# Optimization experiments

Hardware: AMD Instinct MI355X
Metric: run time of the kernel (lower is better)

The kernel has to match this reference:

```python
import jax, jax.numpy as jnp
import numpy as np

N_NODES = 100000
N_EDGES = 1600000
N_FEAT = 16
HIDDEN = 128
N_GRAPHS = 512


def setup_inputs() -> dict:
    key = jax.random.key(0)
    ks = jax.random.split(key, 9)
    x = jax.random.normal(ks[0], (N_NODES, N_FEAT), dtype=jnp.float32)
    edge_index = jax.random.randint(ks[1], (2, N_EDGES), 0, N_NODES, dtype=jnp.int64)
    batch = jnp.sort(jax.random.randint(ks[2], (N_NODES,), 0, N_GRAPHS, dtype=jnp.int64))
    s1 = 1.0 / np.sqrt(N_FEAT)
    s2 = 1.0 / np.sqrt(HIDDEN)
    W1 = jax.random.uniform(ks[3], (N_FEAT, HIDDEN), jnp.float32, -s1, s1)
    b1 = jax.random.uniform(ks[4], (HIDDEN,), jnp.float32, -s1, s1)
    W2 = jax.random.uniform(ks[5], (HIDDEN, HIDDEN), jnp.float32, -s2, s2)
    b2 = jax.random.uniform(ks[6], (HIDDEN,), jnp.float32, -s2, s2)
    Wl = jax.random.uniform(ks[7], (HIDDEN, 1), jnp.float32, -s2, s2)
    bl = jax.random.uniform(ks[8], (1,), jnp.float32, -s2, s2)
    return {"x": x, "edge_index": edge_index, "batch": batch,
            "W1": W1, "b1": b1, "W2": W2, "b2": b2, "Wl": Wl, "bl": bl}


def _gcn_conv(x, W, b, src, dst, n_nodes):
    # PyG GCNConv: h = x @ W; add self-loops; sym-normalized scatter-add; + bias
    h = x @ W  # [N, H]
    deg = jnp.zeros((n_nodes,), h.dtype).at[dst].add(1.0) + 1.0  # self-loop adds 1
    dinv = jax.lax.rsqrt(deg)  # deg >= 1, safe
    norm = dinv[src] * dinv[dst]  # [E]
    out = jnp.zeros_like(h).at[dst].add(h[src] * norm[:, None])
    out = out + h * (dinv * dinv)[:, None]  # self-loop term
    return out + b


def reference(x, edge_index, batch, W1, b1, W2, b2, Wl, bl):
    src, dst = edge_index[0], edge_index[1]
    n = x.shape[0]
    h = jax.nn.relu(_gcn_conv(x, W1, b1, src, dst, n))
    h = jax.nn.relu(_gcn_conv(h, W2, b2, src, dst, n))
    # global_mean_pool over graphs
    sums = jax.ops.segment_sum(h, batch, num_segments=N_GRAPHS)
    counts = jax.ops.segment_sum(jnp.ones((n,), h.dtype), batch, num_segments=N_GRAPHS)
    pooled = sums / jnp.maximum(counts, 1.0)[:, None]  # [G, H]
    return (pooled @ Wl + bl).squeeze(-1)  # [G]
```

## Files before the change

### kernel.cpp

```cpp
#include <hip/hip_runtime.h>
#include <hip/hip_bf16.h>

#define N_NODES 100000
#define N_EDGES 1600000
#define N_FEAT  16
#define HIDDEN  128
#define N_GRAPHS 512
#define CAP     64
#define NBKT    782
#define BN      128
#define CAPB    2560
#define EPB     4000

typedef unsigned short ushort_t;
typedef short v8s __attribute__((ext_vector_type(8)));
typedef float v4f __attribute__((ext_vector_type(4)));

__device__ __forceinline__ ushort_t f2bf(float f) {
    __hip_bfloat16 b = __float2bfloat16(f);
    return *(ushort_t*)&b;
}
__device__ __forceinline__ float bf_lo(unsigned u) {
    union { unsigned i; float f; } c; c.i = u << 16; return c.f;
}
__device__ __forceinline__ float bf_hi(unsigned u) {
    union { unsigned i; float f; } c; c.i = u & 0xffff0000u; return c.f;
}


__global__ __launch_bounds__(256) void k_part(const int* __restrict__ src,
                                              const int* __restrict__ dst,
                                              int* __restrict__ bcnt,
                                              int* __restrict__ ebuf,
                                              const float* __restrict__ W2,
                                              ushort_t* __restrict__ Bp) {
    int tid = threadIdx.x;

    if (blockIdx.x >= N_EDGES / EPB) {
        int idx = (blockIdx.x - N_EDGES / EPB) * 256 + tid;
        int j = idx & 7;
        int lane = (idx >> 3) & 63;
        int nt = (idx >> 9) & 7;
        int kt = idx >> 12;
        int k = kt * 32 + (lane >> 4) * 8 + j;
        int n = nt * 16 + (lane & 15);
        Bp[idx] = f2bf(W2[k * HIDDEN + n]);
        return;
    }

    __shared__ int h[NBKT];
    __shared__ int base[NBKT];
    __shared__ int r[NBKT];
    int e0 = blockIdx.x * EPB;

    for (int i = tid; i < NBKT; i += 256) { h[i] = 0; r[i] = 0; }
    __syncthreads();

    int nloc = (tid < EPB - 15 * 256) ? 16 : 15;
    int v[16], bb[16];
    #pragma unroll
    for (int k = 0; k < 16; ++k) {
        if (k < nloc) {
            int i = e0 + tid + k * 256;
            int s = src[i], d = dst[i];
            bb[k] = d >> 7;
            v[k] = s | ((d & 127) << 17);
            atomicAdd(&h[bb[k]], 1);
        }
    }
    __syncthreads();

    for (int i = tid; i < NBKT; i += 256)
        base[i] = atomicAdd(&bcnt[i], h[i]);
    __syncthreads();

    #pragma unroll
    for (int k = 0; k < 16; ++k) {
        if (k < nloc) {
            int b = bb[k];
            int pos = base[b] + atomicAdd(&r[b], 1);
            if (pos < CAPB) ebuf[b * CAPB + pos] = v[k];
        }
    }
}


__global__ __launch_bounds__(256) void k_fill(const int* __restrict__ bcnt,
                                              const int* __restrict__ ebuf,
                                              const float* __restrict__ x,
                                              int* __restrict__ esrc64,
                                              int* __restrict__ cnt,
                                              float* __restrict__ dinv,
                                              ushort_t* __restrict__ xb,
                                              ushort_t* __restrict__ h1) {
    __shared__ int lcnt[BN];
    int tid = threadIdx.x;
    int b = blockIdx.x;
    int node0 = b << 7;

    if (tid < BN) lcnt[tid] = 0;
    __syncthreads();

    int nE = bcnt[b]; nE = nE > CAPB ? CAPB : nE;
    const int* eb = ebuf + b * CAPB;
    for (int i = tid; i < nE; i += 256) {
        int v = eb[i];
        int dl = v >> 17;
        int p = atomicAdd(&lcnt[dl], 1);
        if (p < CAP) esrc64[((node0 + dl) << 6) + p] = v & 0x1FFFF;
    }
    __syncthreads();

    if (tid < BN) {
        int node = node0 + tid;
        if (node < N_NODES) {
            int c = lcnt[tid];
            cnt[node] = c;
            dinv[node] = rsqrtf((float)c + 1.0f);
            int cc = c > CAP ? CAP : c;
            int pad = (cc + 7) & ~7;
            for (int p = cc; p < pad; ++p)
                esrc64[(node << 6) + p] = N_NODES;
        }
    }

    for (int i = tid; i < BN * N_FEAT; i += 256) {
        int nl = i >> 4;
        int node = node0 + nl;
        if (node < N_NODES) {
            float di = rsqrtf((float)lcnt[nl] + 1.0f);
            xb[node * N_FEAT + (i & 15)] = f2bf(x[node * N_FEAT + (i & 15)] * di);
        }
    }

    if (b == 0) {
        if (tid < N_FEAT) xb[N_NODES * N_FEAT + tid] = 0;
        if (tid < HIDDEN) h1[(size_t)N_NODES * HIDDEN + tid] = 0;
    }
}


__global__ __launch_bounds__(256) void k_agg1f(const int* __restrict__ cnt,
                                               const int* __restrict__ esrc64,
                                               const float* __restrict__ dinv,
                                               const ushort_t* __restrict__ xb,
                                               const float* __restrict__ W1,
                                               const float* __restrict__ b1,
                                               ushort_t* __restrict__ h1) {
    __shared__ float sw[N_FEAT * HIDDEN];
    __shared__ float sx[32][20];
    __shared__ float sdd[32];
    int tid = threadIdx.x;
    for (int i = tid; i < N_FEAT * HIDDEN; i += 256) sw[i] = W1[i];

    int wv = tid >> 6;
    int sub = (tid >> 3) & 7;
    int l8 = tid & 7;
    int nl = wv * 8 + sub;
    int node = blockIdx.x * 32 + nl;
    const unsigned* xr = (const unsigned*)xb;

    int deg = cnt[node]; deg = deg > CAP ? CAP : deg;
    int deg8 = (deg + 7) & ~7;
    int base = node << 6;
    float dd = dinv[node];

    float a0 = 0.0f, a1 = 0.0f;
    for (int j = 0; j < deg8; j += 8) {
        int4 ia = *(const int4*)(esrc64 + base + j);
        int4 ib = *(const int4*)(esrc64 + base + j + 4);
        unsigned u0 = xr[(unsigned)ia.x * 8 + l8];
        unsigned u1 = xr[(unsigned)ia.y * 8 + l8];
        unsigned u2 = xr[(unsigned)ia.z * 8 + l8];
        unsigned u3 = xr[(unsigned)ia.w * 8 + l8];
        unsigned u4 = xr[(unsigned)ib.x * 8 + l8];
        unsigned u5 = xr[(unsigned)ib.y * 8 + l8];
        unsigned u6 = xr[(unsigned)ib.z * 8 + l8];
        unsigned u7 = xr[(unsigned)ib.w * 8 + l8];
        a0 += bf_lo(u0) + bf_lo(u1) + bf_lo(u2) + bf_lo(u3)
            + bf_lo(u4) + bf_lo(u5) + bf_lo(u6) + bf_lo(u7);
        a1 += bf_hi(u0) + bf_hi(u1) + bf_hi(u2) + bf_hi(u3)
            + bf_hi(u4) + bf_hi(u5) + bf_hi(u6) + bf_hi(u7);
    }
    unsigned su = xr[(unsigned)node * 8 + l8];
    a0 = (a0 + bf_lo(su)) * dd;
    a1 = (a1 + bf_hi(su)) * dd;

    sx[nl][2 * l8] = a0;
    sx[nl][2 * l8 + 1] = a1;
    if (l8 == 0) sdd[nl] = dd;
    __syncthreads();

    int f = tid & 127, half = tid >> 7;
    float bias = b1[f];
    float acc[16];
    #pragma unroll
    for (int n = 0; n < 16; ++n) acc[n] = bias;
    #pragma unroll
    for (int k4 = 0; k4 < 4; ++k4) {
        float w0 = sw[(k4 * 4 + 0) * HIDDEN + f];
        float w1 = sw[(k4 * 4 + 1) * HIDDEN + f];
        float w2 = sw[(k4 * 4 + 2) * HIDDEN + f];
        float w3 = sw[(k4 * 4 + 3) * HIDDEN + f];
        #pragma unroll
        for (int n = 0; n < 16; ++n) {
            float4 xv = *(const float4*)(&sx[half * 16 + n][k4 * 4]);
            acc[n] += xv.x * w0 + xv.y * w1 + xv.z * w2 + xv.w * w3;
        }
    }
    int n0 = blockIdx.x * 32 + half * 16;
    #pragma unroll
    for (int n = 0; n < 16; ++n)
        h1[(size_t)(n0 + n) * HIDDEN + f] =
            f2bf(sdd[half * 16 + n] * fmaxf(acc[n], 0.0f));
}


__global__ __launch_bounds__(128) void k_l2(const int* __restrict__ cnt,
                                            const int* __restrict__ esrc64,
                                            const float* __restrict__ dinv,
                                            const ushort_t* __restrict__ h1,
                                            const ushort_t* __restrict__ Bp,
                                            const float* __restrict__ b2,
                                            const float* __restrict__ Wl,
                                            float* __restrict__ snode) {
    __shared__ ushort_t sA[32 * 132];
    int tid = threadIdx.x;
    int wv = tid >> 6, lane = tid & 63;
    int half = lane >> 5, l32 = lane & 31;
    int node0 = blockIdx.x * 32;
    const uint2* h = (const uint2*)h1;

    for (int p = 0; p < 8; ++p) {
        int nl = wv * 16 + p * 2 + half;
        int node = node0 + nl;
        int deg = cnt[node]; deg = deg > CAP ? CAP : deg;
        int deg8 = (deg + 7) & ~7;
        int base = node << 6;
        float dd = dinv[node];
        uint2 sv = h[node * 32 + l32];
        float a0 = bf_lo(sv.x), a1 = bf_hi(sv.x), a2 = bf_lo(sv.y), a3 = bf_hi(sv.y);

        for (int j = 0; j < deg8; j += 8) {
            int4 ia = *(const int4*)(esrc64 + base + j);
            int4 ib = *(const int4*)(esrc64 + base + j + 4);
            uint2 v0 = h[(unsigned)ia.x * 32 + l32];
            uint2 v1 = h[(unsigned)ia.y * 32 + l32];
            uint2 v2 = h[(unsigned)ia.z * 32 + l32];
            uint2 v3 = h[(unsigned)ia.w * 32 + l32];
            uint2 v4 = h[(unsigned)ib.x * 32 + l32];
            uint2 v5 = h[(unsigned)ib.y * 32 + l32];
            uint2 v6 = h[(unsigned)ib.z * 32 + l32];
            uint2 v7 = h[(unsigned)ib.w * 32 + l32];
            a0 += bf_lo(v0.x) + bf_lo(v1.x) + bf_lo(v2.x) + bf_lo(v3.x)
                + bf_lo(v4.x) + bf_lo(v5.x) + bf_lo(v6.x) + bf_lo(v7.x);
            a1 += bf_hi(v0.x) + bf_hi(v1.x) + bf_hi(v2.x) + bf_hi(v3.x)
                + bf_hi(v4.x) + bf_hi(v5.x) + bf_hi(v6.x) + bf_hi(v7.x);
            a2 += bf_lo(v0.y) + bf_lo(v1.y) + bf_lo(v2.y) + bf_lo(v3.y)
                + bf_lo(v4.y) + bf_lo(v5.y) + bf_lo(v6.y) + bf_lo(v7.y);
            a3 += bf_hi(v0.y) + bf_hi(v1.y) + bf_hi(v2.y) + bf_hi(v3.y)
                + bf_hi(v4.y) + bf_hi(v5.y) + bf_hi(v6.y) + bf_hi(v7.y);
        }
        ushort4 r;
        r.x = f2bf(a0 * dd); r.y = f2bf(a1 * dd);
        r.z = f2bf(a2 * dd); r.w = f2bf(a3 * dd);
        *(ushort4*)(&sA[nl * 132 + l32 * 4]) = r;
    }
    __syncthreads();

    int m = lane & 15, quad = lane >> 4;
    const ushort_t* arow = &sA[(wv * 16 + m) * 132];

    v4f acc[8];
    #pragma unroll
    for (int nt = 0; nt < 8; ++nt) acc[nt] = (v4f){0.f, 0.f, 0.f, 0.f};

    #pragma unroll
    for (int kt = 0; kt < 4; ++kt) {
        union { v8s v; ushort4 q[2]; } au;
        au.q[0] = *(const ushort4*)(arow + kt * 32 + quad * 8);
        au.q[1] = *(const ushort4*)(arow + kt * 32 + quad * 8 + 4);
        #pragma unroll
        for (int nt = 0; nt < 8; ++nt) {
            v8s b = *(const v8s*)(Bp + ((kt * 8 + nt) * 64 + lane) * 8);
            acc[nt] = __builtin_amdgcn_mfma_f32_16x16x32_bf16(au.v, b, acc[nt], 0, 0, 0);
        }
    }

    float part[4] = {0, 0, 0, 0};
    #pragma unroll
    for (int nt = 0; nt < 8; ++nt) {
        float bb = b2[nt * 16 + m];
        float wl = Wl[nt * 16 + m];
        #pragma unroll
        for (int reg = 0; reg < 4; ++reg)
            part[reg] += fmaxf(acc[nt][reg] + bb, 0.0f) * wl;
    }
    int node0b = node0 + wv * 16;
    #pragma unroll
    for (int reg = 0; reg < 4; ++reg) {
        float p = part[reg];
        p += __shfl_xor(p, 1, 64);
        p += __shfl_xor(p, 2, 64);
        p += __shfl_xor(p, 4, 64);
        p += __shfl_xor(p, 8, 64);
        int node = node0b + quad * 4 + reg;
        if (m == 0 && node < N_NODES) snode[node] = p;
    }
}


__global__ __launch_bounds__(256) void k_pool(const float* __restrict__ snode,
                                              const int* __restrict__ batch,
                                              const float* __restrict__ bl,
                                              float* __restrict__ out) {
    int g = blockIdx.x;
    int tid = threadIdx.x;
    __shared__ float sred[4];

    int lo = 0, hi = N_NODES;
    while (lo < hi) { int mid = (lo + hi) >> 1; if (batch[mid] < g) lo = mid + 1; else hi = mid; }
    int start = lo;
    hi = N_NODES;
    while (lo < hi) { int mid = (lo + hi) >> 1; if (batch[mid] < g + 1) lo = mid + 1; else hi = mid; }
    int end = lo;

    float acc = 0.0f;
    for (int n = start + tid; n < end; n += 256) acc += snode[n];

    #pragma unroll
    for (int off = 32; off; off >>= 1) acc += __shfl_down(acc, off, 64);
    int wave = tid >> 6, lane = tid & 63;
    if (lane == 0) sred[wave] = acc;
    __syncthreads();
    if (tid == 0) {
        float s = sred[0] + sred[1] + sred[2] + sred[3];
        float cnt = (float)(end - start);
        out[g] = s / fmaxf(cnt, 1.0f) + bl[0];
    }
}


extern "C" void kernel_launch(void* const* d_in, const int* in_sizes, int n_in,
                              void* d_out, int out_size, void* d_ws, size_t ws_size,
                              hipStream_t stream) {
    const float* x    = (const float*)d_in[0];
    const int*   src  = (const int*)d_in[1];
    const int*   dst  = src + N_EDGES;
    const int*   batch= (const int*)d_in[2];
    const float* W1   = (const float*)d_in[3];
    const float* b1   = (const float*)d_in[4];
    const float* W2   = (const float*)d_in[5];
    const float* b2   = (const float*)d_in[6];
    const float* Wl   = (const float*)d_in[7];
    const float* bl   = (const float*)d_in[8];
    float* out = (float*)d_out;

    char* w = (char*)d_ws;
    size_t off = 0;
    auto alloc = [&](size_t bytes) { char* p = w + off; off = (off + bytes + 255) & ~(size_t)255; return p; };

    ushort_t* h1   = (ushort_t*)alloc((size_t)(N_NODES + 1) * HIDDEN * 2);
    int*   ebuf    = (int*)alloc((size_t)NBKT * CAPB * 4);
    ushort_t* xb   = (ushort_t*)alloc((size_t)(N_NODES + 1) * N_FEAT * 2);
    float* dinv    = (float*)alloc(N_NODES * 4);
    float* snode   = (float*)alloc(N_NODES * 4);
    int*   cnt     = (int*)alloc(N_NODES * 4);
    int*   esrc64  = (int*)alloc((size_t)N_NODES * CAP * 4);
    ushort_t* Bp   = (ushort_t*)alloc(16384 * 2);
    int*   bcnt    = (int*)alloc(NBKT * 4);

    hipMemsetAsync(bcnt, 0, NBKT * sizeof(int), stream);
    k_part<<<N_EDGES / EPB + 64, 256, 0, stream>>>(src, dst, bcnt, ebuf, W2, Bp);
    k_fill<<<NBKT, 256, 0, stream>>>(bcnt, ebuf, x, esrc64, cnt, dinv, xb, h1);

    k_agg1f<<<N_NODES / 32, 256, 0, stream>>>(cnt, esrc64, dinv, xb, W1, b1, h1);

    k_l2<<<N_NODES / 32, 128, 0, stream>>>(cnt, esrc64, dinv, h1, Bp, b2, Wl, snode);

    k_pool<<<N_GRAPHS, 256, 0, stream>>>(snode, batch, bl, out);
}
```

Baseline: 225.1 us.

## Split layer-2 gather and MFMA GEMM into separate kernels with LDS-staged weights

Replaces the fused layer-2 kernel, which gathered neighbours into LDS and then ran an MFMA GEMM, with two kernels. The first is a gather kernel that runs one node per 32-thread group and 8 nodes per 256-thread block, writing a bf16 aggregate to a new global buffer. The second is a GEMM kernel that stages the whole packed W2 into LDS and computes the bias, ReLU and Wl dot per node. The aim is more parallelism and latency hiding for the irregular gather, which previously looped over 8 nodes per wave in 128-thread blocks. The cost is an extra global write and read of a 100000x128 bf16 intermediate plus one more kernel launch, and the last GEMM block reads a few rows past the end of that buffer.

```diff
diff --git a/kernel.cpp b/kernel.cpp
--- a/kernel.cpp
+++ b/kernel.cpp
@@ -216,60 +216,70 @@
 }
 
 
-__global__ __launch_bounds__(128) void k_l2(const int* __restrict__ cnt,
-                                            const int* __restrict__ esrc64,
-                                            const float* __restrict__ dinv,
-                                            const ushort_t* __restrict__ h1,
-                                            const ushort_t* __restrict__ Bp,
-                                            const float* __restrict__ b2,
-                                            const float* __restrict__ Wl,
-                                            float* __restrict__ snode) {
-    __shared__ ushort_t sA[32 * 132];
-    int tid = threadIdx.x;
+__global__ __launch_bounds__(256) void k_agg2(const int* __restrict__ cnt,
+                                              const int* __restrict__ esrc64,
+                                              const float* __restrict__ dinv,
+                                              const ushort_t* __restrict__ h1,
+                                              ushort_t* __restrict__ aggb) {
+    int tid = threadIdx.x;
+    int sub = tid >> 5;
+    int l32 = tid & 31;
+    int node = blockIdx.x * 8 + sub;
+    const uint2* h = (const uint2*)h1;
+    int deg = cnt[node]; deg = deg > CAP ? CAP : deg;
+    int deg8 = (deg + 7) & ~7;
+    int base = node << 6;
+    float dd = dinv[node];
+
+    uint2 sv = h[node * 32 + l32];
+    float a0 = bf_lo(sv.x), a1 = bf_hi(sv.x), a2 = bf_lo(sv.y), a3 = bf_hi(sv.y);
+
+    for (int j = 0; j < deg8; j += 8) {
+        int4 ia = *(const int4*)(esrc64 + base + j);
+        int4 ib = *(const int4*)(esrc64 + base + j + 4);
+        uint2 v0 = h[(unsigned)ia.x * 32 + l32];
+        uint2 v1 = h[(unsigned)ia.y * 32 + l32];
+        uint2 v2 = h[(unsigned)ia.z * 32 + l32];
+        uint2 v3 = h[(unsigned)ia.w * 32 + l32];
+        uint2 v4 = h[(unsigned)ib.x * 32 + l32];
+        uint2 v5 = h[(unsigned)ib.y * 32 + l32];
+        uint2 v6 = h[(unsigned)ib.z * 32 + l32];
+        uint2 v7 = h[(unsigned)ib.w * 32 + l32];
+        a0 += bf_lo(v0.x) + bf_lo(v1.x) + bf_lo(v2.x) + bf_lo(v3.x)
+            + bf_lo(v4.x) + bf_lo(v5.x) + bf_lo(v6.x) + bf_lo(v7.x);
+        a1 += bf_hi(v0.x) + bf_hi(v1.x) + bf_hi(v2.x) + bf_hi(v3.x)
+            + bf_hi(v4.x) + bf_hi(v5.x) + bf_hi(v6.x) + bf_hi(v7.x);
+        a2 += bf_lo(v0.y) + bf_lo(v1.y) + bf_lo(v2.y) + bf_lo(v3.y)
+            + bf_lo(v4.y) + bf_lo(v5.y) + bf_lo(v6.y) + bf_lo(v7.y);
+        a3 += bf_hi(v0.y) + bf_hi(v1.y) + bf_hi(v2.y) + bf_hi(v3.y)
+            + bf_hi(v4.y) + bf_hi(v5.y) + bf_hi(v6.y) + bf_hi(v7.y);
+    }
+    ushort4 r;
+    r.x = f2bf(a0 * dd); r.y = f2bf(a1 * dd);
+    r.z = f2bf(a2 * dd); r.w = f2bf(a3 * dd);
+    ((ushort4*)aggb)[node * 32 + l32] = r;
+}
+
+
+__global__ __launch_bounds__(256) void k_mm2m(const ushort_t* __restrict__ A,
+                                              const ushort_t* __restrict__ Bp,
+                                              const float* __restrict__ b2,
+                                              const float* __restrict__ Wl,
+                                              float* __restrict__ snode) {
+    __shared__ ushort_t sB[16384];
+    int tid = threadIdx.x;
+    {
+        const uint4* s = (const uint4*)Bp;
+        uint4* d = (uint4*)sB;
+        #pragma unroll
+        for (int j = 0; j < 8; ++j) d[tid + 256 * j] = s[tid + 256 * j];
+    }
+    __syncthreads();
+
     int wv = tid >> 6, lane = tid & 63;
-    int half = lane >> 5, l32 = lane & 31;
-    int node0 = blockIdx.x * 32;
-    const uint2* h = (const uint2*)h1;
-
-    for (int p = 0; p < 8; ++p) {
-        int nl = wv * 16 + p * 2 + half;
-        int node = node0 + nl;
-        int deg = cnt[node]; deg = deg > CAP ? CAP : deg;
-        int deg8 = (deg + 7) & ~7;
-        int base = node << 6;
-        float dd = dinv[node];
-        uint2 sv = h[node * 32 + l32];
-        float a0 = bf_lo(sv.x), a1 = bf_hi(sv.x), a2 = bf_lo(sv.y), a3 = bf_hi(sv.y);
-
-        for (int j = 0; j < deg8; j += 8) {
-            int4 ia = *(const int4*)(esrc64 + base + j);
-            int4 ib = *(const int4*)(esrc64 + base + j + 4);
-            uint2 v0 = h[(unsigned)ia.x * 32 + l32];
-            uint2 v1 = h[(unsigned)ia.y * 32 + l32];
-            uint2 v2 = h[(unsigned)ia.z * 32 + l32];
-            uint2 v3 = h[(unsigned)ia.w * 32 + l32];
-            uint2 v4 = h[(unsigned)ib.x * 32 + l32];
-            uint2 v5 = h[(unsigned)ib.y * 32 + l32];
-            uint2 v6 = h[(unsigned)ib.z * 32 + l32];
-            uint2 v7 = h[(unsigned)ib.w * 32 + l32];
-            a0 += bf_lo(v0.x) + bf_lo(v1.x) + bf_lo(v2.x) + bf_lo(v3.x)
-                + bf_lo(v4.x) + bf_lo(v5.x) + bf_lo(v6.x) + bf_lo(v7.x);
-            a1 += bf_hi(v0.x) + bf_hi(v1.x) + bf_hi(v2.x) + bf_hi(v3.x)
-                + bf_hi(v4.x) + bf_hi(v5.x) + bf_hi(v6.x) + bf_hi(v7.x);
-            a2 += bf_lo(v0.y) + bf_lo(v1.y) + bf_lo(v2.y) + bf_lo(v3.y)
-                + bf_lo(v4.y) + bf_lo(v5.y) + bf_lo(v6.y) + bf_lo(v7.y);
-            a3 += bf_hi(v0.y) + bf_hi(v1.y) + bf_hi(v2.y) + bf_hi(v3.y)
-                + bf_hi(v4.y) + bf_hi(v5.y) + bf_hi(v6.y) + bf_hi(v7.y);
-        }
-        ushort4 r;
-        r.x = f2bf(a0 * dd); r.y = f2bf(a1 * dd);
-        r.z = f2bf(a2 * dd); r.w = f2bf(a3 * dd);
-        *(ushort4*)(&sA[nl * 132 + l32 * 4]) = r;
-    }
-    __syncthreads();
-
     int m = lane & 15, quad = lane >> 4;
-    const ushort_t* arow = &sA[(wv * 16 + m) * 132];
+    int node0 = blockIdx.x * 64 + wv * 16;
+    const ushort_t* arow = A + (size_t)(node0 + m) * HIDDEN;
 
     v4f acc[8];
     #pragma unroll
@@ -277,13 +287,11 @@
 
     #pragma unroll
     for (int kt = 0; kt < 4; ++kt) {
-        union { v8s v; ushort4 q[2]; } au;
-        au.q[0] = *(const ushort4*)(arow + kt * 32 + quad * 8);
-        au.q[1] = *(const ushort4*)(arow + kt * 32 + quad * 8 + 4);
+        v8s a = *(const v8s*)(arow + kt * 32 + quad * 8);
         #pragma unroll
         for (int nt = 0; nt < 8; ++nt) {
-            v8s b = *(const v8s*)(Bp + ((kt * 8 + nt) * 64 + lane) * 8);
-            acc[nt] = __builtin_amdgcn_mfma_f32_16x16x32_bf16(au.v, b, acc[nt], 0, 0, 0);
+            v8s b = *(const v8s*)(&sB[((kt * 8 + nt) * 64 + lane) * 8]);
+            acc[nt] = __builtin_amdgcn_mfma_f32_16x16x32_bf16(a, b, acc[nt], 0, 0, 0);
         }
     }
 
@@ -296,7 +304,6 @@
         for (int reg = 0; reg < 4; ++reg)
             part[reg] += fmaxf(acc[nt][reg] + bb, 0.0f) * wl;
     }
-    int node0b = node0 + wv * 16;
     #pragma unroll
     for (int reg = 0; reg < 4; ++reg) {
         float p = part[reg];
@@ -304,7 +311,7 @@
         p += __shfl_xor(p, 2, 64);
         p += __shfl_xor(p, 4, 64);
         p += __shfl_xor(p, 8, 64);
-        int node = node0b + quad * 4 + reg;
+        int node = node0 + quad * 4 + reg;
         if (m == 0 && node < N_NODES) snode[node] = p;
     }
 }
@@ -368,6 +375,7 @@
     int*   cnt     = (int*)alloc(N_NODES * 4);
     int*   esrc64  = (int*)alloc((size_t)N_NODES * CAP * 4);
     ushort_t* Bp   = (ushort_t*)alloc(16384 * 2);
+    ushort_t* aggb = (ushort_t*)alloc((size_t)N_NODES * HIDDEN * 2);
     int*   bcnt    = (int*)alloc(NBKT * 4);
 
     hipMemsetAsync(bcnt, 0, NBKT * sizeof(int), stream);
@@ -376,7 +384,8 @@
 
     k_agg1f<<<N_NODES / 32, 256, 0, stream>>>(cnt, esrc64, dinv, xb, W1, b1, h1);
 
-    k_l2<<<N_NODES / 32, 128, 0, stream>>>(cnt, esrc64, dinv, h1, Bp, b2, Wl, snode);
+    k_agg2<<<N_NODES / 8, 256, 0, stream>>>(cnt, esrc64, dinv, h1, aggb);
+    k_mm2m<<<(N_NODES + 63) / 64, 256, 0, stream>>>(aggb, Bp, b2, Wl, snode);
 
     k_pool<<<N_GRAPHS, 256, 0, stream>>>(snode, batch, bl, out);
 }
```

Result: no change. 224.7 us (-0.2%).
